# Performance work log

Measured on AMD Instinct MI355X. Metric: run time of the kernel, lower is better.

The kernel has to match this reference:

```python
import jax, jax.numpy as jnp
import numpy as np

NUM_DENSE = 13
NUM_SPARSE = 26
FEAT_NUM = 40000  # categories per sparse field
FEATURE_LENGTH = NUM_SPARSE * FEAT_NUM + NUM_DENSE  # 1_040_013
K = 64
BATCH = 4096


def setup_inputs() -> dict:
    key = jax.random.key(0)
    k1, k2, k3, k4 = jax.random.split(key, 4)
    dense_inputs = jax.random.normal(k1, (BATCH, NUM_DENSE), dtype=jnp.float32)
    sparse_inputs = jax.random.randint(k2, (BATCH, NUM_SPARSE), 0, FEAT_NUM, dtype=jnp.int64)
    w0 = jnp.zeros((1,), dtype=jnp.float32)
    w = jax.random.normal(k3, (FEATURE_LENGTH, 1), dtype=jnp.float32) * 0.05
    V = jax.random.normal(k4, (K, FEATURE_LENGTH), dtype=jnp.float32) * 0.05
    return {"dense_inputs": dense_inputs, "sparse_inputs": sparse_inputs, "w0": w0, "w": w, "V": V}


def reference(dense_inputs, sparse_inputs, w0, w, V):
    # Feature layout matches the original concat order: [dense (NUM_DENSE) | one-hot field 0 | ... | one-hot field 25].
    # The one-hot @ matrix products are computed as row gathers (mathematically identical,
    # since one_hot(i) @ M == M[i]).
    offsets = NUM_DENSE + FEAT_NUM * jnp.arange(NUM_SPARSE, dtype=sparse_inputs.dtype)
    idx = sparse_inputs + offsets[None, :]  # [B, NUM_SPARSE] global row ids into feature_length

    # ---- first order: w0 + stack @ w ----
    w_dense = w[:NUM_DENSE]            # [ND, 1]
    first = w0 + dense_inputs @ w_dense + jnp.sum(w[idx, 0], axis=1, keepdims=True)  # [B,1]

    # ---- second order: 0.5 * sum((stack @ V^T)^2 - (stack^2 @ (V^T)^2), axis=1) ----
    Vt = V.T                           # [F, K]
    Vt_dense = Vt[:NUM_DENSE]          # [ND, K]
    Vt_sparse = Vt[idx]                # [B, NUM_SPARSE, K] gathered latent vectors

    sv = dense_inputs @ Vt_dense + jnp.sum(Vt_sparse, axis=1)                 # [B, K]
    # stack^2 for the one-hot block equals the one-hot block itself (0/1 entries)
    s2v2 = (dense_inputs ** 2) @ (Vt_dense ** 2) + jnp.sum(Vt_sparse ** 2, axis=1)  # [B, K]

    second = 0.5 * jnp.sum(sv ** 2 - s2v2, axis=1, keepdims=True)  # [B,1]
    return first + second
```

## Files before the change

kernel.cpp:

```cpp
#include <hip/hip_runtime.h>

#define NUM_DENSE 13
#define NUM_SPARSE 26
#define FEAT_NUM 40000
#define FEATURE_LENGTH (NUM_SPARSE * FEAT_NUM + NUM_DENSE)
#define KDIM 64
#define BATCH 4096
#define QSIZE 4000
#define NCHUNK 10
#define LDSN (QSIZE + 4)
#define NT 1024
#define NG 8
#define NBUF 4
#define LA 4

__global__ void transpose_kernel(const int* __restrict__ sp, int* __restrict__ sp_t) {
    int tid = blockIdx.x * blockDim.x + threadIdx.x;
    int j = tid >> 12;
    int b = tid & 4095;
    sp_t[tid] = sp[b * NUM_SPARSE + j];
}

__device__ __forceinline__ float4 gload16(const float4* p) {
    float4 r;
    asm volatile("global_load_dwordx4 %0, %1, off"
                 : "=&v"(r)
                 : "v"((const __attribute__((address_space(1))) float4*)p));
    return r;
}

__device__ __forceinline__ void swrite16(float* lp, float4 v) {
    *reinterpret_cast<float4*>(lp) = v;
}

__global__ __launch_bounds__(NT, 8) void accum_kernel(const float* __restrict__ V,
                                                      const int* __restrict__ sp_t,
                                                      float* __restrict__ PS,
                                                      float* __restrict__ PQ) {
    __shared__ __align__(16) float buf[NBUF][LDSN];

    const int k = blockIdx.x;
    const int g = blockIdx.y;
    const int tid = threadIdx.x;
    const int jstart = (g * NUM_SPARSE) / NG;
    const int jend   = ((g + 1) * NUM_SPARSE) / NG;
    const int nw     = jend - jstart;

    const size_t kbase = (size_t)k * FEATURE_LENGTH + NUM_DENSE;
    const int a   = (int)(kbase & 3);
    const int nl4 = (QSIZE + a + 3) >> 2;
    const int nstage = nw * NCHUNK;

    const float4* g4b = (const float4*)(V + kbase + (size_t)jstart * FEAT_NUM - a) + tid;
    const bool ld = (tid < nl4);

    int s0[4], s1[4], s2[4], s3[4];
#pragma unroll
    for (int r = 0; r < 4; ++r) {
        s0[r] = sp_t[(jstart + 0) * BATCH + tid + NT * r];
        s1[r] = sp_t[(jstart + 1) * BATCH + tid + NT * r];
        s2[r] = sp_t[(jstart + 2) * BATCH + tid + NT * r];
    }
    if (nw == 4) {
#pragma unroll
        for (int r = 0; r < 4; ++r) s3[r] = sp_t[(jstart + 3) * BATCH + tid + NT * r];
    } else {
#pragma unroll
        for (int r = 0; r < 4; ++r) s3[r] = 0;
    }

    float sAcc[4] = {0.f, 0.f, 0.f, 0.f};
    float qAcc[4] = {0.f, 0.f, 0.f, 0.f};
    int cs[4];
#pragma unroll
    for (int r = 0; r < 4; ++r) cs[r] = s0[r];

    __syncthreads();

    float4 R[4];
    if (ld) {
        R[0] = gload16(g4b);
        R[1] = gload16(g4b + 1000);
        R[2] = gload16(g4b + 2000);
        R[3] = gload16(g4b + 3000);
    }
    asm volatile("s_waitcnt vmcnt(3)" ::: "memory");
    if (ld) swrite16(&buf[0][4 * tid], R[0]);

    int wg = 0, qg = 0;
    for (int sb = 0; sb < nstage; sb += 4) {
#pragma unroll
        for (int u = 0; u < 4; ++u) {
            const int s = sb + u;
            if (s < nstage) {
                if (s + LA < nstage && ld)
                    R[u] = gload16(g4b + (size_t)(s + LA) * 1000);
                if (s + 1 < nstage) {
                    const int pend = (nstage - 2 - s < 3) ? (nstage - 2 - s) : 3;
                    if (pend == 3)      asm volatile("s_waitcnt vmcnt(3)" ::: "memory");
                    else if (pend == 2) asm volatile("s_waitcnt vmcnt(2)" ::: "memory");
                    else if (pend == 1) asm volatile("s_waitcnt vmcnt(1)" ::: "memory");
                    else                asm volatile("s_waitcnt vmcnt(0)" ::: "memory");
                    if (ld) swrite16(&buf[(u + 1) & 3][4 * tid], R[(u + 1) & 3]);
                }
                asm volatile("s_waitcnt lgkmcnt(0)" ::: "memory");
                __builtin_amdgcn_s_barrier();
                asm volatile("" ::: "memory");

                const int q0 = qg * QSIZE;
                const float* __restrict__ bb = buf[u];
#pragma unroll
                for (int r = 0; r < 4; ++r) {
                    int rel = cs[r] - q0;
                    bool in = (rel >= 0) && (rel < QSIZE);
                    int addr = in ? (rel + a) : 0;
                    float v = bb[addr];
                    v = in ? v : 0.f;
                    sAcc[r] += v;
                    qAcc[r] += v * v;
                }
                if (++qg == NCHUNK) {
                    qg = 0; ++wg;
                    if (wg < nw) {
#pragma unroll
                        for (int r = 0; r < 4; ++r)
                            cs[r] = (wg == 1) ? s1[r] : (wg == 2) ? s2[r] : s3[r];
                    }
                }
            }
        }
    }

    const int base = (g * KDIM + k) * BATCH + tid;
#pragma unroll
    for (int r = 0; r < 4; ++r) {
        PS[base + NT * r] = sAcc[r];
        PQ[base + NT * r] = qAcc[r];
    }
}

__global__ __launch_bounds__(256) void final_kernel(const float* __restrict__ dense,
                                                    const float* __restrict__ w0,
                                                    const float* __restrict__ w,
                                                    const float* __restrict__ V,
                                                    const int* __restrict__ sp_t,
                                                    const float* __restrict__ PS,
                                                    const float* __restrict__ PQ,
                                                    float* __restrict__ out) {
    __shared__ float red[16][17];
    const int tid = threadIdx.x;
    const int bi  = tid & 15;
    const int ki  = tid >> 4;
    const int b   = blockIdx.x * 16 + bi;

    float x[NUM_DENSE], x2[NUM_DENSE];
#pragma unroll
    for (int d = 0; d < NUM_DENSE; ++d) {
        x[d]  = dense[b * NUM_DENSE + d];
        x2[d] = x[d] * x[d];
    }

    float t = 0.f;
#pragma unroll
    for (int kk = 0; kk < 4; ++kk) {
        const int k = ki * 4 + kk;
        float sv = 0.f, qv = 0.f;
#pragma unroll
        for (int g = 0; g < NG; ++g) {
            sv += PS[((g << 6) + k) * BATCH + b];
            qv += PQ[((g << 6) + k) * BATCH + b];
        }
        const float* __restrict__ Vk = V + (size_t)k * FEATURE_LENGTH;
#pragma unroll
        for (int d = 0; d < NUM_DENSE; ++d) {
            float vv = Vk[d];
            sv += x[d] * vv;
            qv += x2[d] * vv * vv;
        }
        t += sv * sv - qv;
    }
    red[bi][ki] = 0.5f * t;
    __syncthreads();

    if (tid < 16) {
        const int bb = blockIdx.x * 16 + tid;
        float acc = w0[0];
#pragma unroll
        for (int i = 0; i < 16; ++i) acc += red[tid][i];
#pragma unroll
        for (int j = 0; j < NUM_SPARSE; ++j)
            acc += w[NUM_DENSE + j * FEAT_NUM + sp_t[j * BATCH + bb]];
#pragma unroll
        for (int d = 0; d < NUM_DENSE; ++d) acc += x[d] * w[d];
        out[bb] = acc;
    }
}

extern "C" void kernel_launch(void* const* d_in, const int* in_sizes, int n_in,
                              void* d_out, int out_size, void* d_ws, size_t ws_size,
                              hipStream_t stream) {
    const float* dense  = (const float*)d_in[0];
    const int*   sparse = (const int*)d_in[1];
    const float* w0     = (const float*)d_in[2];
    const float* w      = (const float*)d_in[3];
    const float* V      = (const float*)d_in[4];
    float* out = (float*)d_out;

    char* ws = (char*)d_ws;
    int*   sp_t = (int*)ws;
    float* PS   = (float*)(ws + (1 << 20));
    float* PQ   = (float*)(ws + (1 << 20) + NG * KDIM * BATCH * 4);

    transpose_kernel<<<(NUM_SPARSE * BATCH) / 256, 256, 0, stream>>>(sparse, sp_t);
    accum_kernel<<<dim3(KDIM, NG), NT, 0, stream>>>(V, sp_t, PS, PQ);
    final_kernel<<<BATCH / 16, 256, 0, stream>>>(dense, w0, w, V, sp_t, PS, PQ, out);
}
```

Baseline: 389.4 us.

## Prefetch V slabs, reduce partials atomically, and restructure final kernel

Each accum block first streams its whole V slab with fire-and-forget loads and no barriers, so the slab is pulled into cache ahead of the barrier-synchronised LDS pipeline. Per-group partial sums are now combined with atomicAdd into a single PS/PQ buffer instead of NG separate buffers. That buffer is zeroed inside the transpose kernel, which becomes a combined setup kernel. The final kernel handles 64 batch rows per block, stages the dense V columns in LDS and preloads the sparse indices. The cost is that V is read twice, with the second pass relying on cache hits. Float atomics also make the summation order nondeterministic.

```diff
diff --git a/kernel.cpp b/kernel.cpp
--- a/kernel.cpp
+++ b/kernel.cpp
@@ -14,11 +14,14 @@
 #define NBUF 4
 #define LA 4
 
-__global__ void transpose_kernel(const int* __restrict__ sp, int* __restrict__ sp_t) {
-    int tid = blockIdx.x * blockDim.x + threadIdx.x;
-    int j = tid >> 12;
-    int b = tid & 4095;
-    sp_t[tid] = sp[b * NUM_SPARSE + j];
+__global__ void setup_kernel(const int* __restrict__ sp, int* __restrict__ sp_t,
+                             float* __restrict__ Z) {
+    int gid = blockIdx.x * blockDim.x + threadIdx.x;
+    Z[gid] = 0.f;
+    if (gid < NUM_SPARSE * BATCH) {
+        int j = gid >> 12, b = gid & 4095;
+        sp_t[gid] = sp[b * NUM_SPARSE + j];
+    }
 }
 
 __device__ __forceinline__ float4 gload16(const float4* p) {
@@ -76,6 +79,25 @@
     for (int r = 0; r < 4; ++r) cs[r] = s0[r];
 
     __syncthreads();
+
+    if (ld) {
+        int t = 0;
+        for (; t + 4 <= nstage; t += 4) {
+            (void)gload16(g4b + (size_t)(t + 0) * 1000);
+            asm volatile("s_waitcnt vmcnt(3)");
+            (void)gload16(g4b + (size_t)(t + 1) * 1000);
+            asm volatile("s_waitcnt vmcnt(3)");
+            (void)gload16(g4b + (size_t)(t + 2) * 1000);
+            asm volatile("s_waitcnt vmcnt(3)");
+            (void)gload16(g4b + (size_t)(t + 3) * 1000);
+            asm volatile("s_waitcnt vmcnt(3)");
+        }
+        for (; t < nstage; ++t) {
+            (void)gload16(g4b + (size_t)t * 1000);
+            asm volatile("s_waitcnt vmcnt(3)");
+        }
+    }
+    asm volatile("s_waitcnt vmcnt(0)");
 
     float4 R[4];
     if (ld) {
@@ -131,11 +153,11 @@
         }
     }
 
-    const int base = (g * KDIM + k) * BATCH + tid;
+    const int base = k * BATCH + tid;
 #pragma unroll
     for (int r = 0; r < 4; ++r) {
-        PS[base + NT * r] = sAcc[r];
-        PQ[base + NT * r] = qAcc[r];
+        atomicAdd(&PS[base + NT * r], sAcc[r]);
+        atomicAdd(&PQ[base + NT * r], qAcc[r]);
     }
 }
 
@@ -147,11 +169,18 @@
                                                     const float* __restrict__ PS,
                                                     const float* __restrict__ PQ,
                                                     float* __restrict__ out) {
-    __shared__ float red[16][17];
-    const int tid = threadIdx.x;
-    const int bi  = tid & 15;
-    const int ki  = tid >> 4;
-    const int b   = blockIdx.x * 16 + bi;
+    __shared__ float VdL[KDIM][16];
+    __shared__ float red[4][68];
+    const int tid  = threadIdx.x;
+    const int lane = tid & 63;
+    const int wv   = tid >> 6;
+    const int b    = blockIdx.x * 64 + lane;
+
+    for (int i = tid; i < KDIM * 16; i += 256) {
+        int kk = i >> 4, d = i & 15;
+        if (d < NUM_DENSE) VdL[kk][d] = V[(size_t)kk * FEATURE_LENGTH + d];
+    }
+    __syncthreads();
 
     float x[NUM_DENSE], x2[NUM_DENSE];
 #pragma unroll
@@ -160,39 +189,35 @@
         x2[d] = x[d] * x[d];
     }
 
-    float t = 0.f;
-#pragma unroll
-    for (int kk = 0; kk < 4; ++kk) {
-        const int k = ki * 4 + kk;
-        float sv = 0.f, qv = 0.f;
-#pragma unroll
-        for (int g = 0; g < NG; ++g) {
-            sv += PS[((g << 6) + k) * BATCH + b];
-            qv += PQ[((g << 6) + k) * BATCH + b];
-        }
-        const float* __restrict__ Vk = V + (size_t)k * FEATURE_LENGTH;
+    float tt = 0.f;
+#pragma unroll
+    for (int i = 0; i < 16; ++i) {
+        const int kk = wv * 16 + i;
+        float sv = PS[kk * BATCH + b];
+        float qv = PQ[kk * BATCH + b];
 #pragma unroll
         for (int d = 0; d < NUM_DENSE; ++d) {
-            float vv = Vk[d];
+            float vv = VdL[kk][d];
             sv += x[d] * vv;
             qv += x2[d] * vv * vv;
         }
-        t += sv * sv - qv;
-    }
-    red[bi][ki] = 0.5f * t;
+        tt += sv * sv - qv;
+    }
+    red[wv][lane] = tt;
     __syncthreads();
 
-    if (tid < 16) {
-        const int bb = blockIdx.x * 16 + tid;
-        float acc = w0[0];
-#pragma unroll
-        for (int i = 0; i < 16; ++i) acc += red[tid][i];
+    if (tid < 64) {
+        float acc = w0[0] + 0.5f * (red[0][lane] + red[1][lane] +
+                                    red[2][lane] + red[3][lane]);
+        int idx[NUM_SPARSE];
+#pragma unroll
+        for (int j = 0; j < NUM_SPARSE; ++j) idx[j] = sp_t[j * BATCH + b];
 #pragma unroll
         for (int j = 0; j < NUM_SPARSE; ++j)
-            acc += w[NUM_DENSE + j * FEAT_NUM + sp_t[j * BATCH + bb]];
+            acc += w[NUM_DENSE + j * FEAT_NUM + idx[j]];
 #pragma unroll
         for (int d = 0; d < NUM_DENSE; ++d) acc += x[d] * w[d];
-        out[bb] = acc;
+        out[b] = acc;
     }
 }
 
@@ -208,10 +233,11 @@
 
     char* ws = (char*)d_ws;
     int*   sp_t = (int*)ws;
-    float* PS   = (float*)(ws + (1 << 20));
-    float* PQ   = (float*)(ws + (1 << 20) + NG * KDIM * BATCH * 4);
-
-    transpose_kernel<<<(NUM_SPARSE * BATCH) / 256, 256, 0, stream>>>(sparse, sp_t);
+    float* PS   = (float*)(ws + (1 << 19));
+    float* PQ   = (float*)(ws + (1 << 19) + (1 << 20));
+    float* Z    = PS;
+
+    setup_kernel<<<2048, 256, 0, stream>>>(sparse, sp_t, Z);
     accum_kernel<<<dim3(KDIM, NG), NT, 0, stream>>>(V, sp_t, PS, PQ);
-    final_kernel<<<BATCH / 16, 256, 0, stream>>>(dense, w0, w, V, sp_t, PS, PQ, out);
-}
+    final_kernel<<<BATCH / 64, 256, 0, stream>>>(dense, w0, w, V, sp_t, PS, PQ, out);
+}
```

Result: slower. 416.2 us (+6.9%).
